# Performance work log

Measured on AMD Instinct MI355X. Metric: run time of the kernel, lower is better.

## Reference

```python
import jax, jax.numpy as jnp
import numpy as np

B, H, S, D = 4, 16, 2048, 128
HIDDEN_DIM = 128  # init arg; used as softmax scale


def setup_inputs() -> dict:
    key = jax.random.key(0)
    kq, kk, kv = jax.random.split(key, 3)
    q = jax.random.normal(kq, (B, H, S, D), dtype=jnp.float32)
    k = jax.random.normal(kk, (B, H, S, D), dtype=jnp.float32)
    v = jax.random.normal(kv, (B, H, S, D), dtype=jnp.float32)
    return {"q": q, "k": k, "v": v}


def reference(q, k, v):
    # scores[b,h,s,t] = sum_d q[b,h,s,d] * k[b,h,t,d]  (y permuted on last two dims, then matmul)
    scores = jnp.einsum("bhsd,bhtd->bhst", q, k) * (HIDDEN_DIM ** -0.5)
    probs = jax.nn.softmax(scores, axis=-1)
    return jnp.einsum("bhst,bhtd->bhsd", probs, v)
```

## Files before the change

### kernel.cpp

```cpp
#include <hip/hip_runtime.h>
#include <hip/hip_bf16.h>


#define SEQ 2048
#define DH  128
#define NBH 64
#define BM  128
#define BN  64
#define NT  (SEQ / BN)
#define QK_LD 136
#define VT_LD 72
#define P_LD  72
#define THR 8.0f

typedef __attribute__((ext_vector_type(8))) short short8;
typedef __attribute__((ext_vector_type(4))) float f32x4;
typedef __attribute__((ext_vector_type(16))) float f32x16;

#if __has_builtin(__builtin_amdgcn_exp2f)
#define EXP2F(x) __builtin_amdgcn_exp2f(x)
#else
#define EXP2F(x) exp2f(x)
#endif

#define CS (0.08838834764831845f * 1.44269504088896340736f)

__device__ __forceinline__ unsigned int pk_bf16(float lo, float hi) {
    union { __hip_bfloat162 h; unsigned int u; } cv;
    cv.h = __float22bfloat162_rn(make_float2(lo, hi));
    return cv.u;
}

template<bool DOK>
__global__ __launch_bounds__(256) void prep_kernel(
        const float* __restrict__ v, unsigned short* __restrict__ vt,
        const float* __restrict__ k, unsigned short* __restrict__ kb) {
    __shared__ float tile[64][129];
    const int bh  = blockIdx.z;
    const int s0  = blockIdx.x * 64;
    const int tid = threadIdx.x;

    if (DOK) {
        const size_t kbase = ((size_t)blockIdx.x + 32 * (size_t)bh) * 8192;
#pragma unroll
        for (int i = 0; i < 8; ++i) {
            size_t idx = kbase + ((size_t)tid + 256 * i) * 4;
            float4 val = *reinterpret_cast<const float4*>(k + idx);
            uint2 pk;
            pk.x = pk_bf16(val.x, val.y);
            pk.y = pk_bf16(val.z, val.w);
            *reinterpret_cast<uint2*>(kb + idx) = pk;
        }
    }

    const float* src = v + ((size_t)bh * SEQ + s0) * DH;
#pragma unroll
    for (int i = 0; i < 8; ++i) {
        int id  = tid + 256 * i;
        int row = id >> 5;
        int c4  = (id & 31) << 2;
        float4 val = *reinterpret_cast<const float4*>(src + row * DH + c4);
        tile[row][c4 + 0] = val.x;
        tile[row][c4 + 1] = val.y;
        tile[row][c4 + 2] = val.z;
        tile[row][c4 + 3] = val.w;
    }
    __syncthreads();
    unsigned short* dst = vt + (size_t)bh * DH * SEQ + s0;
#pragma unroll
    for (int i = 0; i < 4; ++i) {
        int id = tid + 256 * i;
        int dd = id >> 3;
        int kc = (id & 7) << 3;
        uint4 pk;
        unsigned int* pw = reinterpret_cast<unsigned int*>(&pk);
#pragma unroll
        for (int j = 0; j < 4; ++j)
            pw[j] = pk_bf16(tile[kc + 2 * j][dd], tile[kc + 2 * j + 1][dd]);
        *reinterpret_cast<uint4*>(dst + (size_t)dd * SEQ + kc) = pk;
    }
}

__global__ __launch_bounds__(256, 2) void fattn_kernel(
        const float* __restrict__ q, const unsigned short* __restrict__ kb,
        const unsigned short* __restrict__ vt, float* __restrict__ out) {
    __shared__ unsigned short Ks[BN * QK_LD];
    __shared__ unsigned short Vs[DH * VT_LD];

    const int wid = ((blockIdx.x & 7) << 7) | (blockIdx.x >> 3);
    const int bh  = wid >> 4;
    const int q0  = (wid & 15) * BM;
    const int tid  = threadIdx.x;
    const int w    = tid >> 6;
    const int lane = tid & 63;
    const int l31  = lane & 31;
    const int hi   = lane >> 5;

    short8 qb[8];
    {
        const float* qptr = q + ((size_t)bh * SEQ + q0 + w * 32 + l31) * DH + hi * 8;
#pragma unroll
        for (int ks = 0; ks < 8; ++ks) {
            float4 x = *reinterpret_cast<const float4*>(qptr + 16 * ks);
            float4 y = *reinterpret_cast<const float4*>(qptr + 16 * ks + 4);
            union { short8 s; uint4 u; } cv;
            cv.u.x = pk_bf16(x.x * CS, x.y * CS);
            cv.u.y = pk_bf16(x.z * CS, x.w * CS);
            cv.u.z = pk_bf16(y.x * CS, y.y * CS);
            cv.u.w = pk_bf16(y.z * CS, y.w * CS);
            qb[ks] = cv.s;
        }
    }

    f32x16 o0, o1, o2, o3;
#pragma unroll
    for (int i = 0; i < 16; ++i) { o0[i] = 0.f; o1[i] = 0.f; o2[i] = 0.f; o3[i] = 0.f; }
    float m = -1e30f, lsum = 0.f;

    const unsigned short* kbp  = kb + (size_t)bh * SEQ * DH;
    const unsigned short* vptr = vt + (size_t)bh * DH * SEQ;

    uint4 kr0, kr1, kr2, kr3, vr0, vr1, vr2, vr3;
    const int krow = tid >> 4, kcol = (tid & 15) << 3;
    const int vrow = tid >> 3, vcol = (tid & 7) << 3;
    const unsigned short* kst = kbp + (size_t)krow * DH + kcol;
    const unsigned short* vst = vptr + (size_t)vrow * SEQ + vcol;

#define LOAD_TILE(K0)                                                              \
    do {                                                                           \
        const unsigned short* _kp = kst + (size_t)(K0) * DH;                       \
        kr0 = *reinterpret_cast<const uint4*>(_kp);                                \
        kr1 = *reinterpret_cast<const uint4*>(_kp + 16 * DH);                      \
        kr2 = *reinterpret_cast<const uint4*>(_kp + 32 * DH);                      \
        kr3 = *reinterpret_cast<const uint4*>(_kp + 48 * DH);                      \
        const unsigned short* _vp = vst + (K0);                                    \
        vr0 = *reinterpret_cast<const uint4*>(_vp);                                \
        vr1 = *reinterpret_cast<const uint4*>(_vp + 32 * SEQ);                     \
        vr2 = *reinterpret_cast<const uint4*>(_vp + 64 * SEQ);                     \
        vr3 = *reinterpret_cast<const uint4*>(_vp + 96 * SEQ);                     \
    } while (0)

#define WRITE_TILE()                                                               \
    do {                                                                           \
        *reinterpret_cast<uint4*>(&Ks[(krow     ) * QK_LD + kcol]) = kr0;          \
        *reinterpret_cast<uint4*>(&Ks[(krow + 16) * QK_LD + kcol]) = kr1;          \
        *reinterpret_cast<uint4*>(&Ks[(krow + 32) * QK_LD + kcol]) = kr2;          \
        *reinterpret_cast<uint4*>(&Ks[(krow + 48) * QK_LD + kcol]) = kr3;          \
        *reinterpret_cast<uint4*>(&Vs[(vrow     ) * VT_LD + vcol]) = vr0;          \
        *reinterpret_cast<uint4*>(&Vs[(vrow + 32) * VT_LD + vcol]) = vr1;          \
        *reinterpret_cast<uint4*>(&Vs[(vrow + 64) * VT_LD + vcol]) = vr2;          \
        *reinterpret_cast<uint4*>(&Vs[(vrow + 96) * VT_LD + vcol]) = vr3;          \
    } while (0)

    LOAD_TILE(0);
    WRITE_TILE();
    __syncthreads();

    const unsigned short* KsA = &Ks[l31 * QK_LD + hi * 8];
    const unsigned short* VsA = &Vs[l31 * VT_LD + hi * 8];

    for (int kt = 0; kt < NT; ++kt) {
        f32x16 s0, s1;
#pragma unroll
        for (int i = 0; i < 16; ++i) { s0[i] = 0.f; s1[i] = 0.f; }
        __builtin_amdgcn_s_setprio(1);
#pragma unroll
        for (int ks = 0; ks < 8; ++ks) {
            short8 a0 = *reinterpret_cast<const short8*>(KsA + 16 * ks);
            short8 a1 = *reinterpret_cast<const short8*>(KsA + 32 * QK_LD + 16 * ks);
            s0 = __builtin_amdgcn_mfma_f32_32x32x16_bf16(a0, qb[ks], s0, 0, 0, 0);
            s1 = __builtin_amdgcn_mfma_f32_32x32x16_bf16(a1, qb[ks], s1, 0, 0, 0);
        }
        __builtin_amdgcn_s_setprio(0);

        float mx = s0[0];
#pragma unroll
        for (int i = 1; i < 16; ++i) mx = fmaxf(mx, s0[i]);
#pragma unroll
        for (int i = 0; i < 16; ++i) mx = fmaxf(mx, s1[i]);
        mx = fmaxf(mx, __shfl_xor(mx, 32));
        if (__any(mx - m > THR)) {
            float mn = fmaxf(m, mx);
            float al = EXP2F(m - mn);
            m = mn; lsum *= al;
#pragma unroll
            for (int i = 0; i < 16; ++i) { o0[i] *= al; o1[i] *= al; o2[i] *= al; o3[i] *= al; }
        }
#pragma unroll
        for (int i = 0; i < 16; ++i) s0[i] = EXP2F(s0[i] - m);
#pragma unroll
        for (int i = 0; i < 16; ++i) s1[i] = EXP2F(s1[i] - m);
        float ls = 0.f;
#pragma unroll
        for (int i = 0; i < 16; ++i) ls += s0[i] + s1[i];
        lsum += ls;

        short8 pf0, pf1, pf2, pf3;
#define MAKE_PF(PF, SG, S)                                                         \
        {                                                                          \
            unsigned pq0 = pk_bf16(SG[8*(S)+0], SG[8*(S)+1]);                      \
            unsigned pq1 = pk_bf16(SG[8*(S)+2], SG[8*(S)+3]);                      \
            unsigned pq2 = pk_bf16(SG[8*(S)+4], SG[8*(S)+5]);                      \
            unsigned pq3 = pk_bf16(SG[8*(S)+6], SG[8*(S)+7]);                      \
            unsigned px0 = (unsigned)__shfl_xor((int)pq0, 32);                     \
            unsigned px1 = (unsigned)__shfl_xor((int)pq1, 32);                     \
            unsigned px2 = (unsigned)__shfl_xor((int)pq2, 32);                     \
            unsigned px3 = (unsigned)__shfl_xor((int)pq3, 32);                     \
            union { short8 s; uint4 u; } cv;                                       \
            cv.u.x = hi ? px2 : pq0;                                               \
            cv.u.y = hi ? px3 : pq1;                                               \
            cv.u.z = hi ? pq2 : px0;                                               \
            cv.u.w = hi ? pq3 : px1;                                               \
            PF = cv.s;                                                             \
        }
        MAKE_PF(pf0, s0, 0)
        MAKE_PF(pf1, s0, 1)
        MAKE_PF(pf2, s1, 0)
        MAKE_PF(pf3, s1, 1)

        if (kt + 1 < NT) LOAD_TILE((kt + 1) * BN);

        __builtin_amdgcn_s_setprio(1);
#define PV_C(OC, C)                                                                \
        {                                                                          \
            short8 va0 = *reinterpret_cast<const short8*>(VsA + (32*(C)) * VT_LD);      \
            short8 va1 = *reinterpret_cast<const short8*>(VsA + (32*(C)) * VT_LD + 16); \
            short8 va2 = *reinterpret_cast<const short8*>(VsA + (32*(C)) * VT_LD + 32); \
            short8 va3 = *reinterpret_cast<const short8*>(VsA + (32*(C)) * VT_LD + 48); \
            OC = __builtin_amdgcn_mfma_f32_32x32x16_bf16(va0, pf0, OC, 0, 0, 0);   \
            OC = __builtin_amdgcn_mfma_f32_32x32x16_bf16(va1, pf1, OC, 0, 0, 0);   \
            OC = __builtin_amdgcn_mfma_f32_32x32x16_bf16(va2, pf2, OC, 0, 0, 0);   \
            OC = __builtin_amdgcn_mfma_f32_32x32x16_bf16(va3, pf3, OC, 0, 0, 0);   \
        }
        PV_C(o0, 0) PV_C(o1, 1) PV_C(o2, 2) PV_C(o3, 3)
        __builtin_amdgcn_s_setprio(0);

        __syncthreads();
        if (kt + 1 < NT) WRITE_TILE();
        __syncthreads();
    }

    lsum += __shfl_xor(lsum, 32);
    float inv = 1.0f / lsum;
    float* obase = out + ((size_t)bh * SEQ + q0 + w * 32 + l31) * DH + 4 * hi;
#define STORE_C(OC, C)                                                             \
    {                                                                              \
        _Pragma("unroll")                                                          \
        for (int u = 0; u < 4; ++u) {                                              \
            float4 st;                                                             \
            st.x = OC[4*u+0] * inv; st.y = OC[4*u+1] * inv;                        \
            st.z = OC[4*u+2] * inv; st.w = OC[4*u+3] * inv;                        \
            *reinterpret_cast<float4*>(obase + 32*(C) + 8*u) = st;                 \
        }                                                                          \
    }
    STORE_C(o0, 0) STORE_C(o1, 1) STORE_C(o2, 2) STORE_C(o3, 3)
}

__global__ __launch_bounds__(256, 3) void fattn_fallback(
        const float* __restrict__ q, const float* __restrict__ kf,
        const unsigned short* __restrict__ vt, float* __restrict__ out) {
    __shared__ unsigned short Ks[64 * QK_LD];
    __shared__ unsigned short Vs[DH * VT_LD];
    __shared__ unsigned short Ps[64 * P_LD];

    const int wid = ((blockIdx.x & 7) << 8) | (blockIdx.x >> 3);
    const int bh  = wid >> 5;
    const int q0  = (wid & 31) * 64;
    const int tid  = threadIdx.x;
    const int w    = tid >> 6;
    const int lane = tid & 63;
    const int l15  = lane & 15;
    const int quad = lane >> 4;

    short8 qf[4];
    {
        const float* qptr = q + ((size_t)bh * SEQ + q0 + w * 16 + l15) * DH + quad * 8;
#pragma unroll
        for (int kk = 0; kk < 4; ++kk) {
            float4 x = *reinterpret_cast<const float4*>(qptr + kk * 32);
            float4 y = *reinterpret_cast<const float4*>(qptr + kk * 32 + 4);
            union { short8 s; uint4 u; } cv;
            cv.u.x = pk_bf16(x.x * CS, x.y * CS);
            cv.u.y = pk_bf16(x.z * CS, x.w * CS);
            cv.u.z = pk_bf16(y.x * CS, y.y * CS);
            cv.u.w = pk_bf16(y.z * CS, y.w * CS);
            qf[kk] = cv.s;
        }
    }

    f32x4 o[8];
#pragma unroll
    for (int t = 0; t < 8; ++t) o[t] = (f32x4){0.f, 0.f, 0.f, 0.f};
    float mrow[4] = {-1e30f, -1e30f, -1e30f, -1e30f};
    float lrow[4] = {0.f, 0.f, 0.f, 0.f};

    const float*          kfp  = kf + (size_t)bh * SEQ * DH;
    const unsigned short* vptr = vt + (size_t)bh * DH * SEQ;

    unsigned int* Ps32 = reinterpret_cast<unsigned int*>(Ps);
    const int prow_base = w * 16 + quad * 4;
    const int pdw = (l15 & 1) ? (8 + (l15 >> 1)) : (l15 >> 1);

    for (int kt = 0; kt < NT; ++kt) {
        const int k0 = kt * BN;
#pragma unroll
        for (int i = 0; i < 8; ++i) {
            int id  = tid + 256 * i;
            int row = id >> 5;
            int c4  = (id & 31) << 2;
            float4 val = *reinterpret_cast<const float4*>(kfp + (size_t)(k0 + row) * DH + c4);
            uint2 pk;
            pk.x = pk_bf16(val.x, val.y);
            pk.y = pk_bf16(val.z, val.w);
            *reinterpret_cast<uint2*>(&Ks[row * QK_LD + c4]) = pk;
        }
#pragma unroll
        for (int i = 0; i < 4; ++i) {
            int id = tid + 256 * i;
            int dd = id >> 3;
            int kc = (id & 7) << 3;
            *reinterpret_cast<uint4*>(&Vs[dd * VT_LD + kc]) =
                *reinterpret_cast<const uint4*>(vptr + (size_t)dd * SEQ + k0 + kc);
        }
        __syncthreads();

        f32x4 acc[4];
#pragma unroll
        for (int t = 0; t < 4; ++t) acc[t] = (f32x4){0.f, 0.f, 0.f, 0.f};
#pragma unroll
        for (int kk = 0; kk < 4; ++kk) {
            const int koff = kk * 32 + quad * 8;
#pragma unroll
            for (int t = 0; t < 4; ++t) {
                short8 b = *reinterpret_cast<const short8*>(&Ks[(t * 16 + l15) * QK_LD + koff]);
                acc[t] = __builtin_amdgcn_mfma_f32_16x16x32_bf16(qf[kk], b, acc[t], 0, 0, 0);
            }
        }

        float lm[4];
#pragma unroll
        for (int r = 0; r < 4; ++r)
            lm[r] = fmaxf(fmaxf(acc[0][r], acc[1][r]), fmaxf(acc[2][r], acc[3][r]));
        float need = fmaxf(fmaxf(lm[0] - mrow[0], lm[1] - mrow[1]),
                           fmaxf(lm[2] - mrow[2], lm[3] - mrow[3]));
        if (__any(need > THR)) {
#pragma unroll
            for (int r = 0; r < 4; ++r) {
                float mx = lm[r];
#pragma unroll
                for (int off = 1; off < 16; off <<= 1)
                    mx = fmaxf(mx, __shfl_xor(mx, off));
                float mnew  = fmaxf(mrow[r], mx);
                float alpha = EXP2F(mrow[r] - mnew);
                mrow[r] = mnew;
                lrow[r] *= alpha;
#pragma unroll
                for (int t = 0; t < 8; ++t) o[t][r] *= alpha;
            }
        }

#pragma unroll
        for (int r = 0; r < 4; ++r) {
            float p0 = EXP2F(acc[0][r] - mrow[r]);
            float p1 = EXP2F(acc[1][r] - mrow[r]);
            float p2 = EXP2F(acc[2][r] - mrow[r]);
            float p3 = EXP2F(acc[3][r] - mrow[r]);
            lrow[r] += (p0 + p1) + (p2 + p3);
            unsigned int a01 = pk_bf16(p0, p1);
            unsigned int a23 = pk_bf16(p2, p3);
            unsigned int s01 = __shfl_xor((int)a01, 1);
            unsigned int s23 = __shfl_xor((int)a23, 1);
            unsigned int w0, w1;
            if (l15 & 1) {
                w0 = (s01 >> 16) | (a01 & 0xffff0000u);
                w1 = (s23 >> 16) | (a23 & 0xffff0000u);
            } else {
                w0 = (a01 & 0xffffu) | (s01 << 16);
                w1 = (a23 & 0xffffu) | (s23 << 16);
            }
            const int dw = (prow_base + r) * (P_LD / 2) + pdw;
            Ps32[dw]      = w0;
            Ps32[dw + 16] = w1;
        }

#pragma unroll
        for (int kk = 0; kk < 2; ++kk) {
            const int koff = kk * 32 + quad * 8;
            short8 a = *reinterpret_cast<const short8*>(&Ps[(w * 16 + l15) * P_LD + koff]);
#pragma unroll
            for (int t = 0; t < 8; ++t) {
                short8 b = *reinterpret_cast<const short8*>(&Vs[(t * 16 + l15) * VT_LD + koff]);
                o[t] = __builtin_amdgcn_mfma_f32_16x16x32_bf16(a, b, o[t], 0, 0, 0);
            }
        }
        __syncthreads();
    }

#pragma unroll
    for (int r = 0; r < 4; ++r) {
#pragma unroll
        for (int off = 1; off < 16; off <<= 1)
            lrow[r] += __shfl_xor(lrow[r], off);
    }
    float* obase = out + ((size_t)bh * SEQ + q0) * DH;
#pragma unroll
    for (int r = 0; r < 4; ++r) {
        float inv = 1.0f / lrow[r];
        int row = w * 16 + quad * 4 + r;
#pragma unroll
        for (int t = 0; t < 8; ++t)
            obase[(size_t)row * DH + t * 16 + l15] = o[t][r] * inv;
    }
}

extern "C" void kernel_launch(void* const* d_in, const int* in_sizes, int n_in,
                              void* d_out, int out_size, void* d_ws, size_t ws_size,
                              hipStream_t stream) {
    const float* q = (const float*)d_in[0];
    const float* k = (const float*)d_in[1];
    const float* v = (const float*)d_in[2];
    float* out = (float*)d_out;
    unsigned short* vt = (unsigned short*)d_ws;

    const size_t vt_elems = (size_t)NBH * SEQ * DH;
    if (ws_size >= 2 * vt_elems * sizeof(unsigned short)) {
        unsigned short* kbuf = vt + vt_elems;
        prep_kernel<true><<<dim3(SEQ / 64, 1, NBH), dim3(256), 0, stream>>>(v, vt, k, kbuf);
        fattn_kernel<<<dim3((SEQ / BM) * NBH), dim3(256), 0, stream>>>(q, kbuf, vt, out);
    } else {
        prep_kernel<false><<<dim3(SEQ / 64, 1, NBH), dim3(256), 0, stream>>>(v, vt, nullptr, nullptr);
        fattn_fallback<<<dim3((SEQ / 64) * NBH), dim3(256), 0, stream>>>(q, k, vt, out);
    }
}
```

Before: 364.4 us.

## Double-buffer K/V shared tiles, prefetch earlier, use permlane32_swap for P repack

```diff
diff --git a/kernel.cpp b/kernel.cpp
--- a/kernel.cpp
+++ b/kernel.cpp
@@ -16,6 +16,7 @@
 typedef __attribute__((ext_vector_type(8))) short short8;
 typedef __attribute__((ext_vector_type(4))) float f32x4;
 typedef __attribute__((ext_vector_type(16))) float f32x16;
+typedef __attribute__((ext_vector_type(2))) unsigned int u32x2;
 
 #if __has_builtin(__builtin_amdgcn_exp2f)
 #define EXP2F(x) __builtin_amdgcn_exp2f(x)
@@ -29,6 +30,32 @@
     union { __hip_bfloat162 h; unsigned int u; } cv;
     cv.h = __float22bfloat162_rn(make_float2(lo, hi));
     return cv.u;
+}
+
+__device__ __forceinline__ short8 repack_pf(float a0, float a1, float a2, float a3,
+                                            float a4, float a5, float a6, float a7,
+                                            int hi) {
+    unsigned pq0 = pk_bf16(a0, a1);
+    unsigned pq1 = pk_bf16(a2, a3);
+    unsigned pq2 = pk_bf16(a4, a5);
+    unsigned pq3 = pk_bf16(a6, a7);
+    union { short8 s; uint4 u; } cv;
+#if __has_builtin(__builtin_amdgcn_permlane32_swap)
+    u32x2 r02 = __builtin_amdgcn_permlane32_swap(pq0, pq2, false, false);
+    u32x2 r13 = __builtin_amdgcn_permlane32_swap(pq1, pq3, false, false);
+    cv.u.x = r02[0]; cv.u.y = r13[0]; cv.u.z = r02[1]; cv.u.w = r13[1];
+    (void)hi;
+#else
+    unsigned px0 = (unsigned)__shfl_xor((int)pq0, 32);
+    unsigned px1 = (unsigned)__shfl_xor((int)pq1, 32);
+    unsigned px2 = (unsigned)__shfl_xor((int)pq2, 32);
+    unsigned px3 = (unsigned)__shfl_xor((int)pq3, 32);
+    cv.u.x = hi ? px2 : pq0;
+    cv.u.y = hi ? px3 : pq1;
+    cv.u.z = hi ? pq2 : px0;
+    cv.u.w = hi ? pq3 : px1;
+#endif
+    return cv.s;
 }
 
 template<bool DOK>
@@ -84,8 +111,8 @@
 __global__ __launch_bounds__(256, 2) void fattn_kernel(
         const float* __restrict__ q, const unsigned short* __restrict__ kb,
         const unsigned short* __restrict__ vt, float* __restrict__ out) {
-    __shared__ unsigned short Ks[BN * QK_LD];
-    __shared__ unsigned short Vs[DH * VT_LD];
+    __shared__ unsigned short Ks[2][BN * QK_LD];
+    __shared__ unsigned short Vs[2][DH * VT_LD];
 
     const int wid = ((blockIdx.x & 7) << 7) | (blockIdx.x >> 3);
     const int bh  = wid >> 4;
@@ -140,26 +167,29 @@
         vr3 = *reinterpret_cast<const uint4*>(_vp + 96 * SEQ);                     \
     } while (0)
 
-#define WRITE_TILE()                                                               \
+#define WRITE_TILE(B)                                                              \
     do {                                                                           \
-        *reinterpret_cast<uint4*>(&Ks[(krow     ) * QK_LD + kcol]) = kr0;          \
-        *reinterpret_cast<uint4*>(&Ks[(krow + 16) * QK_LD + kcol]) = kr1;          \
-        *reinterpret_cast<uint4*>(&Ks[(krow + 32) * QK_LD + kcol]) = kr2;          \
-        *reinterpret_cast<uint4*>(&Ks[(krow + 48) * QK_LD + kcol]) = kr3;          \
-        *reinterpret_cast<uint4*>(&Vs[(vrow     ) * VT_LD + vcol]) = vr0;          \
-        *reinterpret_cast<uint4*>(&Vs[(vrow + 32) * VT_LD + vcol]) = vr1;          \
-        *reinterpret_cast<uint4*>(&Vs[(vrow + 64) * VT_LD + vcol]) = vr2;          \
-        *reinterpret_cast<uint4*>(&Vs[(vrow + 96) * VT_LD + vcol]) = vr3;          \
+        *reinterpret_cast<uint4*>(&Ks[B][(krow     ) * QK_LD + kcol]) = kr0;       \
+        *reinterpret_cast<uint4*>(&Ks[B][(krow + 16) * QK_LD + kcol]) = kr1;       \
+        *reinterpret_cast<uint4*>(&Ks[B][(krow + 32) * QK_LD + kcol]) = kr2;       \
+        *reinterpret_cast<uint4*>(&Ks[B][(krow + 48) * QK_LD + kcol]) = kr3;       \
+        *reinterpret_cast<uint4*>(&Vs[B][(vrow     ) * VT_LD + vcol]) = vr0;       \
+        *reinterpret_cast<uint4*>(&Vs[B][(vrow + 32) * VT_LD + vcol]) = vr1;       \
+        *reinterpret_cast<uint4*>(&Vs[B][(vrow + 64) * VT_LD + vcol]) = vr2;       \
+        *reinterpret_cast<uint4*>(&Vs[B][(vrow + 96) * VT_LD + vcol]) = vr3;       \
     } while (0)
 
     LOAD_TILE(0);
-    WRITE_TILE();
+    WRITE_TILE(0);
     __syncthreads();
-
-    const unsigned short* KsA = &Ks[l31 * QK_LD + hi * 8];
-    const unsigned short* VsA = &Vs[l31 * VT_LD + hi * 8];
+    int cur = 0;
 
     for (int kt = 0; kt < NT; ++kt) {
+        if (kt + 1 < NT) LOAD_TILE((kt + 1) * BN);
+
+        const unsigned short* KsA = &Ks[cur][l31 * QK_LD + hi * 8];
+        const unsigned short* VsA = &Vs[cur][l31 * VT_LD + hi * 8];
+
         f32x16 s0, s1;
 #pragma unroll
         for (int i = 0; i < 16; ++i) { s0[i] = 0.f; s1[i] = 0.f; }
@@ -195,30 +225,10 @@
         for (int i = 0; i < 16; ++i) ls += s0[i] + s1[i];
         lsum += ls;
 
-        short8 pf0, pf1, pf2, pf3;
-#define MAKE_PF(PF, SG, S)                                                         \
-        {                                                                          \
-            unsigned pq0 = pk_bf16(SG[8*(S)+0], SG[8*(S)+1]);                      \
-            unsigned pq1 = pk_bf16(SG[8*(S)+2], SG[8*(S)+3]);                      \
-            unsigned pq2 = pk_bf16(SG[8*(S)+4], SG[8*(S)+5]);                      \
-            unsigned pq3 = pk_bf16(SG[8*(S)+6], SG[8*(S)+7]);                      \
-            unsigned px0 = (unsigned)__shfl_xor((int)pq0, 32);                     \
-            unsigned px1 = (unsigned)__shfl_xor((int)pq1, 32);                     \
-            unsigned px2 = (unsigned)__shfl_xor((int)pq2, 32);                     \
-            unsigned px3 = (unsigned)__shfl_xor((int)pq3, 32);                     \
-            union { short8 s; uint4 u; } cv;                                       \
-            cv.u.x = hi ? px2 : pq0;                                               \
-            cv.u.y = hi ? px3 : pq1;                                               \
-            cv.u.z = hi ? pq2 : px0;                                               \
-            cv.u.w = hi ? pq3 : px1;                                               \
-            PF = cv.s;                                                             \
-        }
-        MAKE_PF(pf0, s0, 0)
-        MAKE_PF(pf1, s0, 1)
-        MAKE_PF(pf2, s1, 0)
-        MAKE_PF(pf3, s1, 1)
-
-        if (kt + 1 < NT) LOAD_TILE((kt + 1) * BN);
+        short8 pf0 = repack_pf(s0[0], s0[1], s0[2],  s0[3],  s0[4],  s0[5],  s0[6],  s0[7],  hi);
+        short8 pf1 = repack_pf(s0[8], s0[9], s0[10], s0[11], s0[12], s0[13], s0[14], s0[15], hi);
+        short8 pf2 = repack_pf(s1[0], s1[1], s1[2],  s1[3],  s1[4],  s1[5],  s1[6],  s1[7],  hi);
+        short8 pf3 = repack_pf(s1[8], s1[9], s1[10], s1[11], s1[12], s1[13], s1[14], s1[15], hi);
 
         __builtin_amdgcn_s_setprio(1);
 #define PV_C(OC, C)                                                                \
@@ -235,9 +245,9 @@
         PV_C(o0, 0) PV_C(o1, 1) PV_C(o2, 2) PV_C(o3, 3)
         __builtin_amdgcn_s_setprio(0);
 
+        if (kt + 1 < NT) WRITE_TILE(cur ^ 1);
         __syncthreads();
-        if (kt + 1 < NT) WRITE_TILE();
-        __syncthreads();
+        cur ^= 1;
     }
 
     lsum += __shfl_xor(lsum, 32);
```

New measurement: 352.3 us. -3.3%, faster.
